# Kernel optimization log

Hardware: AMD Instinct MI355X
Metric: run time of the kernel (lower is better)

Reference implementation:

```python
import jax, jax.numpy as jnp
import numpy as np

D = 128      # d_model
H = 8        # n_heads
HD = D // H  # head_dim = 16
E = 256      # n_experts
R = 32       # kv_lora_rank
B, T = 4, 512
EPS = 1e-6


def _dense_init(k, fi, fo):
    s = float(1.0 / np.sqrt(fi))
    return jax.random.uniform(k, (fi, fo), minval=-s, maxval=s, dtype=jnp.float32)


def setup_inputs() -> dict:
    key = jax.random.key(0)
    ks = jax.random.split(key, 16)
    rng = np.random.RandomState(42)
    Q, _ = np.linalg.qr(rng.randn(D, D))
    glim = float(np.sqrt(6.0 / (D + D)))
    return {
        'x': jax.random.normal(ks[0], (B, T, D), dtype=jnp.float32),
        'g1': jnp.ones((D,), jnp.float32),
        'qW': _dense_init(ks[1], D, D), 'qb': jnp.zeros((D,), jnp.float32),
        'kdW': _dense_init(ks[2], D, R), 'kdb': jnp.zeros((R,), jnp.float32),
        'kuW': _dense_init(ks[3], R, 2 * D), 'kub': jnp.zeros((2 * D,), jnp.float32),
        'oW': _dense_init(ks[4], D, D), 'ob': jnp.zeros((D,), jnp.float32),
        'rot': jnp.asarray(Q, jnp.float32),
        'tq_scale': jnp.ones((D,), jnp.float32),
        's1W': _dense_init(ks[5], D, D), 's1b': jnp.zeros((D,), jnp.float32),
        's2W': _dense_init(ks[6], D, D), 's2b': jnp.zeros((D,), jnp.float32),
        'g2': jnp.ones((D,), jnp.float32),
        'gateW': _dense_init(ks[7], D, E), 'gateb': jnp.zeros((E,), jnp.float32),
        'expW': jax.random.uniform(ks[8], (E, D, D), minval=-glim, maxval=glim, dtype=jnp.float32),
        'm1W': _dense_init(ks[9], D, D), 'm1b': jnp.zeros((D,), jnp.float32),
        'm2W': _dense_init(ks[10], D, D), 'm2b': jnp.zeros((D,), jnp.float32),
    }


def _rmsnorm(x, g):
    return g * (x / jnp.sqrt(jnp.mean(x * x, axis=-1, keepdims=True) + EPS))


def _swiglu(x, w1, b1, w2, b2):
    gate = x @ w1 + b1
    return gate * jax.nn.sigmoid(gate) * (x @ w2 + b2)


def _mla(x, qW, qb, kdW, kdb, kuW, kub, oW, ob):
    b, t = x.shape[0], x.shape[1]
    q = (x @ qW + qb).reshape(b, t, H, HD)
    kv = ((x @ kdW + kdb) @ kuW + kub).reshape(b, t, H, 2 * HD)
    k, v = jnp.split(kv, 2, axis=-1)
    q = jax.nn.elu(q) + 1.0
    k = jax.nn.elu(k) + 1.0
    # linear attention: context[b,h,d,e] = sum_t k[b,t,h,d] v[b,t,h,e]
    context = jnp.einsum('bthd,bthe->bhde', k, v)
    out = jnp.einsum('bthd,bhde->bthe', q, context)
    k_sum = jnp.sum(k, axis=1)  # [b,h,d]
    z = 1.0 / (jnp.einsum('bthd,bhd->bth', q, k_sum) + EPS)
    out = out * z[..., None]
    return out.reshape(b, t, D) @ oW + ob


def _turbo_quant(x, rot, scale):
    x = x @ rot
    mag = jnp.sqrt(jnp.mean(x * x, axis=-1, keepdims=True) + EPS)
    phase = x / mag
    qp = jnp.clip(phase * 127.0, -127.0, 127.0) / 127.0
    phase = jax.lax.stop_gradient(qp - phase) + phase  # straight-through
    return phase * mag * scale


def _moe(h, gateW, gateb, expW, m1W, m1b, m2W, m2b):
    gate_scores = jax.nn.softmax(h @ gateW + gateb, axis=-1)  # [B,T,E]
    top_vals, top_idx = jax.lax.top_k(gate_scores, 2)
    top_w = top_vals / (jnp.sum(top_vals, axis=-1, keepdims=True) + EPS)
    # dense all-expert compute as in the original module
    eo = jnp.einsum('btd,edo->bteo', h, expW)  # [B,T,E,D]
    mask = jnp.sum(jax.nn.one_hot(top_idx, E, dtype=h.dtype) * top_w[..., None], axis=2)  # [B,T,E]
    wavg = jnp.einsum('bteo,bte->bto', eo, mask)
    wavg = _swiglu(wavg, m1W, m1b, m2W, m2b)
    diff_sq = jnp.square(eo - wavg[:, :, None, :])
    wvar = jnp.einsum('bteo,bte->bto', diff_sq, mask)
    consensus = jnp.exp(-jnp.mean(wvar, axis=-1))  # [B,T]
    return wavg, consensus


def reference(x, g1, qW, qb, kdW, kdb, kuW, kub, oW, ob, rot, tq_scale,
              s1W, s1b, s2W, s2b, g2, gateW, gateb, expW, m1W, m1b, m2W, m2b):
    attn_out = _turbo_quant(_mla(_rmsnorm(x, g1), qW, qb, kdW, kdb, kuW, kub, oW, ob), rot, tq_scale)
    x = x + _swiglu(attn_out, s1W, s1b, s2W, s2b)
    moe_out, consensus = _moe(_rmsnorm(x, g2), gateW, gateb, expW, m1W, m1b, m2W, m2b)
    return x + moe_out, consensus
```

## Files before the change

### kernel.cpp

```cpp
#include <hip/hip_runtime.h>
#include <math.h>

static constexpr int Dd    = 128;
static constexpr int NH    = 8;
static constexpr int NE    = 256;
static constexpr int RR    = 32;
static constexpr int TT    = 512;
static constexpr int NTOK  = 2048;
static constexpr int SLOTS = 256;
#define EPSF 1e-6f

static constexpr int FD_CTX   = 0;
static constexpr int FD_ROUTE = 4;
static constexpr int FD_EXP   = 5;
static constexpr int NFLAGS   = 261;

__device__ __forceinline__ float elu1(float v) { return v > 0.f ? v + 1.f : expf(v); }
__device__ __forceinline__ float sigm(float v) { return 1.f / (1.f + expf(-v)); }

__device__ __forceinline__ void flag_add(int* p) {
  __hip_atomic_fetch_add(p, 1, __ATOMIC_RELEASE, __HIP_MEMORY_SCOPE_AGENT);
}
__device__ __forceinline__ void flag_wait(int* p, int tgt) {
  int c = 0;
  while (__hip_atomic_load(p, __ATOMIC_ACQUIRE, __HIP_MEMORY_SCOPE_AGENT) < tgt) {
    __builtin_amdgcn_s_sleep(2);
    if (++c > (1 << 27)) break;
  }
}

__global__ __launch_bounds__(512) void k_pre(
    const float* __restrict__ x, const float* __restrict__ g1,
    const float* __restrict__ qW, const float* __restrict__ qb,
    const float* __restrict__ kdW, const float* __restrict__ kdb,
    const float* __restrict__ kuW, const float* __restrict__ kub,
    const float* __restrict__ oW, const float* __restrict__ ob,
    const float* __restrict__ rot,
    float* __restrict__ qbuf, float* __restrict__ kvbuf,
    float* __restrict__ ctx, float* __restrict__ ksum,
    int* __restrict__ cnt, int* __restrict__ flags,
    float* __restrict__ oR, float* __restrict__ bR) {
  const int tid = threadIdx.x;
  const int bid = blockIdx.x;
  const int j = tid & 127, g = tid >> 7;
  const int lane = tid & 63;
  const int n0 = bid * 4;

  __shared__ float4 h1T[128];
  __shared__ float4 part[3][128];
  __shared__ float4 kpart[8][32];
  __shared__ float4 kdT[32];
  __shared__ float4 kupart[256];
  __shared__ float4 rtmp[2];

  if (bid == 0) {
    for (int i = tid; i < 32 * 256; i += 512) ctx[i] = 0.f;
    ksum[tid] = 0.f;
    if (tid < NE) cnt[tid] = 0;
    if (tid < NFLAGS) flags[tid] = 0;
  }

  float xv[4];
  if (tid < 128) {
    float v[4];
#pragma unroll
    for (int t = 0; t < 4; t++) { xv[t] = x[(n0 + t) * Dd + j]; v[t] = xv[t] * xv[t]; }
#pragma unroll
    for (int o = 32; o > 0; o >>= 1) {
#pragma unroll
      for (int t = 0; t < 4; t++) v[t] += __shfl_xor(v[t], o, 64);
    }
    if (lane == 0) rtmp[tid >> 6] = make_float4(v[0], v[1], v[2], v[3]);
  }
  __syncthreads();
  if (tid < 128) {
    float g1j = g1[j];
#pragma unroll
    for (int t = 0; t < 4; t++) {
      float ss = ((const float*)&rtmp[0])[t] + ((const float*)&rtmp[1])[t];
      ((float*)&h1T[j])[t] = g1j * xv[t] * rsqrtf(ss * (1.f / 128.f) + EPSF);
    }
  }
  __syncthreads();

  {
    float a0 = 0, a1 = 0, a2 = 0, a3 = 0;
    const float* Wp = qW + (g * 32) * Dd + j;
#pragma unroll 16
    for (int i = 0; i < 32; i++) {
      float4 h4 = h1T[g * 32 + i];
      float w = Wp[i * Dd];
      a0 += h4.x * w; a1 += h4.y * w; a2 += h4.z * w; a3 += h4.w * w;
    }
    if (g) part[g - 1][j] = make_float4(a0, a1, a2, a3);
    __syncthreads();
    if (g == 0) {
      float4 p0 = part[0][j], p1 = part[1][j], p2 = part[2][j];
      float bb = qb[j];
      qbuf[(n0 + 0) * Dd + j] = elu1(a0 + p0.x + p1.x + p2.x + bb);
      qbuf[(n0 + 1) * Dd + j] = elu1(a1 + p0.y + p1.y + p2.y + bb);
      qbuf[(n0 + 2) * Dd + j] = elu1(a2 + p0.z + p1.z + p2.z + bb);
      qbuf[(n0 + 3) * Dd + j] = elu1(a3 + p0.w + p1.w + p2.w + bb);
    }
    __syncthreads();
  }

  if (tid < 256) {
    int col = tid & 31, ksp = tid >> 5;
    float a0 = 0, a1 = 0, a2 = 0, a3 = 0;
    const float* Wp = kdW + (ksp * 16) * RR + col;
#pragma unroll
    for (int i = 0; i < 16; i++) {
      float4 h4 = h1T[ksp * 16 + i];
      float w = Wp[i * RR];
      a0 += h4.x * w; a1 += h4.y * w; a2 += h4.z * w; a3 += h4.w * w;
    }
    kpart[ksp][col] = make_float4(a0, a1, a2, a3);
  }
  __syncthreads();
  if (tid < 32) {
    float bb = kdb[tid];
    float s0 = bb, s1 = bb, s2 = bb, s3 = bb;
#pragma unroll
    for (int k = 0; k < 8; k++) {
      float4 p = kpart[k][tid];
      s0 += p.x; s1 += p.y; s2 += p.z; s3 += p.w;
    }
    kdT[tid] = make_float4(s0, s1, s2, s3);
  }
  __syncthreads();

  {
    int col = tid & 255, kh = tid >> 8;
    float a0 = 0, a1 = 0, a2 = 0, a3 = 0;
    const float* Wp = kuW + (kh * 16) * 256 + col;
#pragma unroll
    for (int r = 0; r < 16; r++) {
      float4 k4 = kdT[kh * 16 + r];
      float w = Wp[r * 256];
      a0 += k4.x * w; a1 += k4.y * w; a2 += k4.z * w; a3 += k4.w * w;
    }
    if (kh) kupart[col] = make_float4(a0, a1, a2, a3);
    __syncthreads();
    if (!kh) {
      float4 p = kupart[col];
      float bb = kub[col];
      bool isk = (col & 31) < 16;
      float v0 = a0 + p.x + bb, v1 = a1 + p.y + bb, v2 = a2 + p.z + bb, v3 = a3 + p.w + bb;
      kvbuf[(n0 + 0) * 256 + col] = isk ? elu1(v0) : v0;
      kvbuf[(n0 + 1) * 256 + col] = isk ? elu1(v1) : v1;
      kvbuf[(n0 + 2) * 256 + col] = isk ? elu1(v2) : v2;
      kvbuf[(n0 + 3) * 256 + col] = isk ? elu1(v3) : v3;
    }
  }

  if (bid < 32) {
    int idx = bid * 512 + tid;
    int row = idx >> 7, col = idx & 127;
    const float* ow = oW + row * 128;
    float acc = 0.f;
#pragma unroll 8
    for (int k = 0; k < 128; k++) acc += ow[k] * rot[k * 128 + col];
    oR[idx] = acc;
  } else if (bid == 32 && tid < 128) {
    float acc = 0.f;
#pragma unroll 8
    for (int k = 0; k < 128; k++) acc += ob[k] * rot[k * 128 + tid];
    bR[tid] = acc;
  }
}

struct RParams {
  const float *x, *qbuf, *kvbuf, *oR, *bR, *tqs;
  const float *s1W, *s1b, *s2W, *s2b, *g2, *gateW, *gateb, *expW;
  const float *m1W, *m1b, *m2W, *m2b;
  float *ctx, *ksum, *h2buf, *ybuf, *out;
  int *cnt, *slottok, *flags;
};

__global__ __launch_bounds__(512, 4) void k_rest(RParams P) {
  const int tid = threadIdx.x;
  const int bid = blockIdx.x;
  const int j = tid & 127, g = tid >> 7;
  const int lane = tid & 63;
  const int n0 = bid * 4;
  const int b = bid >> 7;

  __shared__ float sh[64 * 32];
  __shared__ float4 bufA[128], bufB[128];
  __shared__ float4 part[3][128];
  __shared__ float4 gpart[256];
  __shared__ float4 rtmp[2];
  __shared__ float wvS[4][4]; __shared__ int wiS[4][4];
  __shared__ float zS[4][4];
  __shared__ int sE[4][2]; __shared__ int sSlot[4][2]; __shared__ float sWt[4][2];
  __shared__ __align__(16) float hT[128 * 20];
  __shared__ float4 y1T[128], y2T[128], inT[128], sT[128];

  float xres[4];
  if (tid < 128) {
#pragma unroll
    for (int t = 0; t < 4; t++) xres[t] = P.x[(n0 + t) * Dd + j];
  }
  ((float*)&bufA[j])[g] = P.qbuf[(n0 + g) * Dd + j];

  if (bid < 256) {
    const int bh = bid >> 3, c = bid & 7;
    const int bb = bh >> 3, h = bh & 7;
#pragma unroll
    for (int r = 0; r < 4; r++) {
      int lin = r * 512 + tid;
      int tok = lin >> 5, off = lin & 31;
      sh[lin] = P.kvbuf[((bb * TT + c * 64 + tok) * 256) + h * 32 + off];
    }
    __syncthreads();
    if (tid < 256) {
      const int d = tid >> 4, e = tid & 15;
      float acc = 0.f, ks = 0.f;
#pragma unroll 4
      for (int t = 0; t < 64; t++) {
        float kk = sh[t * 32 + d];
        acc += kk * sh[t * 32 + 16 + e];
        ks += kk;
      }
      atomicAdd(&P.ctx[bh * 256 + d * 16 + e], acc);
      if (e == 0) atomicAdd(&P.ksum[bh * 16 + d], ks);
    }
    __threadfence();
    __syncthreads();
    if (tid == 0) flag_add(&P.flags[FD_CTX + bb]);
  }

  if (tid == 0) flag_wait(&P.flags[FD_CTX + b], 64);
  __syncthreads();
  __threadfence();

  if (tid < 128) {
    int h = j >> 4, e = j & 15;
    const float* cpt = P.ctx + (b * NH + h) * 256;
    const float* kpt = P.ksum + (b * NH + h) * 16;
    float num[4] = {0, 0, 0, 0}, den[4] = {0, 0, 0, 0};
#pragma unroll
    for (int d = 0; d < 16; d++) {
      float cx = cpt[d * 16 + e], ks = kpt[d];
      float4 q4 = bufA[h * 16 + d];
      num[0] += q4.x * cx; num[1] += q4.y * cx; num[2] += q4.z * cx; num[3] += q4.w * cx;
      den[0] += q4.x * ks; den[1] += q4.y * ks; den[2] += q4.z * ks; den[3] += q4.w * ks;
    }
#pragma unroll
    for (int t = 0; t < 4; t++) ((float*)&bufB[j])[t] = num[t] / (den[t] + EPSF);
  }
  __syncthreads();

  {
    float a0 = 0, a1 = 0, a2 = 0, a3 = 0;
    const float* Wp = P.oR + (g * 32) * Dd + j;
#pragma unroll 16
    for (int i = 0; i < 32; i++) {
      float4 h4 = bufB[g * 32 + i];
      float w = Wp[i * Dd];
      a0 += h4.x * w; a1 += h4.y * w; a2 += h4.z * w; a3 += h4.w * w;
    }
    if (g) part[g - 1][j] = make_float4(a0, a1, a2, a3);
    __syncthreads();
    float tot[4];
    if (g == 0) {
      float4 p0 = part[0][j], p1 = part[1][j], p2 = part[2][j];
      float bb = P.bR[j];
      tot[0] = a0 + p0.x + p1.x + p2.x + bb; tot[1] = a1 + p0.y + p1.y + p2.y + bb;
      tot[2] = a2 + p0.z + p1.z + p2.z + bb; tot[3] = a3 + p0.w + p1.w + p2.w + bb;
      float v[4];
#pragma unroll
      for (int t = 0; t < 4; t++) v[t] = tot[t] * tot[t];
#pragma unroll
      for (int o = 32; o > 0; o >>= 1) {
#pragma unroll
        for (int t = 0; t < 4; t++) v[t] += __shfl_xor(v[t], o, 64);
      }
      if (lane == 0) rtmp[tid >> 6] = make_float4(v[0], v[1], v[2], v[3]);
    }
    __syncthreads();
    if (g == 0) {
      float scj = P.tqs[j];
#pragma unroll
      for (int t = 0; t < 4; t++) {
        float ss = ((const float*)&rtmp[0])[t] + ((const float*)&rtmp[1])[t];
        float mag = sqrtf(ss * (1.f / 128.f) + EPSF);
        float zc = fminf(fmaxf(tot[t], -mag), mag);
        ((float*)&bufA[j])[t] = zc * scj;
      }
    }
    __syncthreads();
  }

  float xn[4] = {0.f, 0.f, 0.f, 0.f};
  {
    float a0 = 0, a1 = 0, a2 = 0, a3 = 0;
    const float* Wp = (g < 2 ? P.s1W : P.s2W) + ((g & 1) * 64) * Dd + j;
#pragma unroll 16
    for (int i = 0; i < 64; i++) {
      float4 h4 = bufA[(g & 1) * 64 + i];
      float w = Wp[i * Dd];
      a0 += h4.x * w; a1 += h4.y * w; a2 += h4.z * w; a3 += h4.w * w;
    }
    if (g) part[g - 1][j] = make_float4(a0, a1, a2, a3);
    __syncthreads();
    if (g == 0) {
      float b1 = P.s1b[j], b2 = P.s2b[j];
      float4 p0 = part[0][j], p1 = part[1][j], p2 = part[2][j];
      float gv[4], uv[4], v[4];
      gv[0] = a0 + p0.x + b1; gv[1] = a1 + p0.y + b1;
      gv[2] = a2 + p0.z + b1; gv[3] = a3 + p0.w + b1;
      uv[0] = p1.x + p2.x + b2; uv[1] = p1.y + p2.y + b2;
      uv[2] = p1.z + p2.z + b2; uv[3] = p1.w + p2.w + b2;
      float g2j = P.g2[j];
#pragma unroll
      for (int t = 0; t < 4; t++) {
        xn[t] = xres[t] + gv[t] * sigm(gv[t]) * uv[t];
        ((float*)&bufB[j])[t] = g2j * xn[t];
        v[t] = xn[t] * xn[t];
      }
#pragma unroll
      for (int o = 32; o > 0; o >>= 1) {
#pragma unroll
        for (int t = 0; t < 4; t++) v[t] += __shfl_xor(v[t], o, 64);
      }
      if (lane == 0) rtmp[tid >> 6] = make_float4(v[0], v[1], v[2], v[3]);
    }
    __syncthreads();
  }

  float val[4]; float r2v[4];
  {
    int col = tid & 255, kh = tid >> 8;
    float a0 = 0, a1 = 0, a2 = 0, a3 = 0;
    const float* Wp = P.gateW + (kh * 64) * NE + col;
#pragma unroll 16
    for (int i = 0; i < 64; i++) {
      float4 h4 = bufB[kh * 64 + i];
      float w = Wp[i * NE];
      a0 += h4.x * w; a1 += h4.y * w; a2 += h4.z * w; a3 += h4.w * w;
    }
    if (kh) gpart[col] = make_float4(a0, a1, a2, a3);
    __syncthreads();
#pragma unroll
    for (int t = 0; t < 4; t++) {
      float ss = ((const float*)&rtmp[0])[t] + ((const float*)&rtmp[1])[t];
      r2v[t] = rsqrtf(ss * (1.f / 128.f) + EPSF);
    }
    if (!kh) {
      float4 p = gpart[col];
      float bb = P.gateb[col];
      val[0] = (a0 + p.x) * r2v[0] + bb; val[1] = (a1 + p.y) * r2v[1] + bb;
      val[2] = (a2 + p.z) * r2v[2] + bb; val[3] = (a3 + p.w) * r2v[3] + bb;
    }
    if (tid < 128) {
#pragma unroll
      for (int t = 0; t < 4; t++)
        P.h2buf[(n0 + t) * Dd + j] = ((const float*)&bufB[j])[t] * r2v[t];
    }
  }
  __syncthreads();

  float m1[4]; int i1[4];
  {
    if (tid < 256) {
      float bv[4]; int bi[4];
#pragma unroll
      for (int t = 0; t < 4; t++) { bv[t] = val[t]; bi[t] = tid; }
#pragma unroll
      for (int o = 32; o > 0; o >>= 1) {
#pragma unroll
        for (int t = 0; t < 4; t++) {
          float wv = __shfl_xor(bv[t], o, 64);
          int wi = __shfl_xor(bi[t], o, 64);
          if (wv > bv[t] || (wv == bv[t] && wi < bi[t])) { bv[t] = wv; bi[t] = wi; }
        }
      }
      if (lane == 0) {
#pragma unroll
        for (int t = 0; t < 4; t++) { wvS[tid >> 6][t] = bv[t]; wiS[tid >> 6][t] = bi[t]; }
      }
    }
    __syncthreads();
    if (tid < 256) {
#pragma unroll
// ... 34 lines not shown
    __syncthreads();
    if (tid < 256) {
#pragma unroll
      for (int t = 0; t < 4; t++) {
        m2[t] = wvS[0][t]; i2[t] = wiS[0][t];
#pragma unroll
        for (int w = 1; w < 4; w++) {
          float cv = wvS[w][t]; int ci = wiS[w][t];
          if (cv > m2[t] || (cv == m2[t] && ci < i2[t])) { m2[t] = cv; i2[t] = ci; }
        }
      }
    }
    __syncthreads();
  }
  {
    if (tid < 256) {
      float v[4];
#pragma unroll
      for (int t = 0; t < 4; t++) v[t] = expf(val[t] - m1[t]);
#pragma unroll
      for (int o = 32; o > 0; o >>= 1) {
#pragma unroll
        for (int t = 0; t < 4; t++) v[t] += __shfl_xor(v[t], o, 64);
      }
      if (lane == 0) {
#pragma unroll
        for (int t = 0; t < 4; t++) zS[tid >> 6][t] = v[t];
      }
    }
    __syncthreads();
  }
  if (tid < 4) {
    int t = tid, tok = n0 + t;
    float Z = zS[0][t] + zS[1][t] + zS[2][t] + zS[3][t];
    float p1 = 1.f / Z;
    float p2 = expf(m2[t] - m1[t]) / Z;
    float s = p1 + p2 + EPSF;
    int e1 = i1[t], e2 = i2[t];
    int s1 = atomicAdd(&P.cnt[e1], 1); if (s1 > SLOTS - 1) s1 = SLOTS - 1;
    int s2 = atomicAdd(&P.cnt[e2], 1); if (s2 > SLOTS - 1) s2 = SLOTS - 1;
    int sl1 = e1 * SLOTS + s1, sl2 = e2 * SLOTS + s2;
    P.slottok[sl1] = tok; P.slottok[sl2] = tok;
    sE[t][0] = e1; sE[t][1] = e2;
    sSlot[t][0] = sl1; sSlot[t][1] = sl2;
    sWt[t][0] = p1 / s; sWt[t][1] = p2 / s;
  }

  __threadfence();
  __syncthreads();
  if (tid == 0) {
    flag_add(&P.flags[FD_ROUTE]);
    flag_wait(&P.flags[FD_ROUTE], 512);
  }
  __syncthreads();
  __threadfence();

  {
    const int e = bid >> 1, sub = bid & 1;
    int n = __hip_atomic_load(&P.cnt[e], __ATOMIC_RELAXED, __HIP_MEMORY_SCOPE_AGENT);
    if (n > SLOTS) n = SLOTS;
    const int base = e * SLOTS;
    const float* Wp = P.expW + (size_t)e * Dd * Dd + j;
    for (int t0 = sub * 16; t0 < n; t0 += 32) {
      int m = n - t0; if (m > 16) m = 16;
      __syncthreads();
      for (int tt = g; tt < m; tt += 4) {
        int tok = P.slottok[base + t0 + tt];
        hT[j * 20 + tt] = P.h2buf[tok * Dd + j];
      }
      __syncthreads();
      float acc[4] = {0, 0, 0, 0};
#pragma unroll 8
      for (int i = 0; i < 128; i++) {
        float w = Wp[i * Dd];
        float4 h4 = *(const float4*)&hT[i * 20 + g * 4];
        acc[0] += h4.x * w; acc[1] += h4.y * w; acc[2] += h4.z * w; acc[3] += h4.w * w;
      }
#pragma unroll
      for (int k = 0; k < 4; k++) {
        int tt = g * 4 + k;
        if (tt < m) P.ybuf[(size_t)(base + t0 + tt) * Dd + j] = acc[k];
      }
    }
    __threadfence();
    __syncthreads();
    if (tid == 0) flag_add(&P.flags[FD_EXP + e]);
  }

  if (tid < 8) {
    int t = tid >> 1, sl = tid & 1;
    flag_wait(&P.flags[FD_EXP + sE[t][sl]], 2);
  }
  __syncthreads();
  __threadfence();

  {
    float y1 = P.ybuf[(size_t)sSlot[g][0] * Dd + j];
    float y2 = P.ybuf[(size_t)sSlot[g][1] * Dd + j];
    ((float*)&y1T[j])[g] = y1;
    ((float*)&y2T[j])[g] = y2;
    ((float*)&inT[j])[g] = sWt[g][0] * y1 + sWt[g][1] * y2;
  }
  __syncthreads();

  {
    float a0 = 0, a1 = 0, a2 = 0, a3 = 0;
    const float* Wp = (g < 2 ? P.m1W : P.m2W) + ((g & 1) * 64) * Dd + j;
#pragma unroll 16
    for (int i = 0; i < 64; i++) {
      float4 h4 = inT[(g & 1) * 64 + i];
      float w = Wp[i * Dd];
      a0 += h4.x * w; a1 += h4.y * w; a2 += h4.z * w; a3 += h4.w * w;
    }
    if (g) part[g - 1][j] = make_float4(a0, a1, a2, a3);
    __syncthreads();
    if (g == 0) {
      float b1 = P.m1b[j], b2 = P.m2b[j];
      float4 p0 = part[0][j], p1 = part[1][j], p2 = part[2][j];
      float gv[4], uv[4];
      gv[0] = a0 + p0.x + b1; gv[1] = a1 + p0.y + b1;
      gv[2] = a2 + p0.z + b1; gv[3] = a3 + p0.w + b1;
      uv[0] = p1.x + p2.x + b2; uv[1] = p1.y + p2.y + b2;
      uv[2] = p1.z + p2.z + b2; uv[3] = p1.w + p2.w + b2;
#pragma unroll
      for (int t = 0; t < 4; t++) {
        float sv = gv[t] * sigm(gv[t]) * uv[t];
        ((float*)&sT[j])[t] = sv;
        P.out[(n0 + t) * Dd + j] = xn[t] + sv;
      }
    }
    __syncthreads();
  }

  if (tid < 128) {
    float v[4];
#pragma unroll
    for (int t = 0; t < 4; t++) {
      float sv = ((const float*)&sT[j])[t];
      float d1 = ((const float*)&y1T[j])[t] - sv;
      float d2 = ((const float*)&y2T[j])[t] - sv;
      v[t] = sWt[t][0] * d1 * d1 + sWt[t][1] * d2 * d2;
    }
#pragma unroll
    for (int o = 32; o > 0; o >>= 1) {
#pragma unroll
      for (int t = 0; t < 4; t++) v[t] += __shfl_xor(v[t], o, 64);
    }
    if (lane == 0) rtmp[tid >> 6] = make_float4(v[0], v[1], v[2], v[3]);
  }
  __syncthreads();
  if (tid < 4) {
    float s = ((const float*)&rtmp[0])[tid] + ((const float*)&rtmp[1])[tid];
    P.out[NTOK * Dd + n0 + tid] = expf(-s * (1.f / 128.f));
  }
}

__global__ __launch_bounds__(256) void k_ctx_fb(const float* __restrict__ kv,
                                                float* __restrict__ ctx,
                                                float* __restrict__ ksum) {
  const int blk = blockIdx.x;
  const int tid = threadIdx.x;
  const int bh = blk >> 3, c = blk & 7;
  const int b = bh >> 3, h = bh & 7;
  const int d = tid >> 4, e = tid & 15;
  __shared__ float sh[64 * 32];
#pragma unroll
  for (int r = 0; r < 8; r++) {
    int lin = r * 256 + tid;
    int tok = lin >> 5, off = lin & 31;
    sh[lin] = kv[((b * TT + c * 64 + tok) * 256) + h * 32 + off];
  }
  __syncthreads();
  float acc = 0.f, ks = 0.f;
#pragma unroll 4
  for (int t = 0; t < 64; t++) {
    float kk = sh[t * 32 + d];
    acc += kk * sh[t * 32 + 16 + e];
    ks += kk;
  }
  atomicAdd(&ctx[bh * 256 + d * 16 + e], acc);
  if (e == 0) atomicAdd(&ksum[bh * 16 + d], ks);
}

__global__ __launch_bounds__(512) void k_mid_fb(
    const float* __restrict__ x, const float* __restrict__ qbuf,
    const float* __restrict__ ctx, const float* __restrict__ ksum,
    const float* __restrict__ oR, const float* __restrict__ bR,
    const float* __restrict__ tqs,
    const float* __restrict__ s1W, const float* __restrict__ s1b,
    const float* __restrict__ s2W, const float* __restrict__ s2b,
    const float* __restrict__ g2, const float* __restrict__ gateW,
    const float* __restrict__ gateb,
    float* __restrict__ xnbuf, float* __restrict__ h2buf,
    float* __restrict__ gw, int* __restrict__ tokslot,
    int* __restrict__ slottok, int* __restrict__ cnt) {
  const int tid = threadIdx.x;
  const int j = tid & 127, g = tid >> 7;
  const int lane = tid & 63;
  const int n0 = blockIdx.x * 4;
  const int b = n0 >> 9;

  __shared__ float4 bufA[128], bufB[128];
  __shared__ float4 part[3][128];
  __shared__ float4 gpart[256];
  __shared__ float4 rtmp[2];
  __shared__ float wvS[4][4]; __shared__ int wiS[4][4];
  __shared__ float zS[4][4];

  float xres[4];
  if (tid < 128) {
#pragma unroll
    for (int t = 0; t < 4; t++) xres[t] = x[(n0 + t) * Dd + j];
  }
  ((float*)&bufA[j])[g] = qbuf[(n0 + g) * Dd + j];
  __syncthreads();

  if (tid < 128) {
    int h = j >> 4, e = j & 15;
    const float* cpt = ctx + (b * NH + h) * 256;
    const float* kpt = ksum + (b * NH + h) * 16;
    float num[4] = {0, 0, 0, 0}, den[4] = {0, 0, 0, 0};
#pragma unroll
    for (int d = 0; d < 16; d++) {
      float cx = cpt[d * 16 + e], ks = kpt[d];
      float4 q4 = bufA[h * 16 + d];
      num[0] += q4.x * cx; num[1] += q4.y * cx; num[2] += q4.z * cx; num[3] += q4.w * cx;
      den[0] += q4.x * ks; den[1] += q4.y * ks; den[2] += q4.z * ks; den[3] += q4.w * ks;
    }
#pragma unroll
    for (int t = 0; t < 4; t++) ((float*)&bufB[j])[t] = num[t] / (den[t] + EPSF);
  }
  __syncthreads();

  {
    float a0 = 0, a1 = 0, a2 = 0, a3 = 0;
    const float* Wp = oR + (g * 32) * Dd + j;
#pragma unroll 16
    for (int i = 0; i < 32; i++) {
      float4 h4 = bufB[g * 32 + i];
      float w = Wp[i * Dd];
      a0 += h4.x * w; a1 += h4.y * w; a2 += h4.z * w; a3 += h4.w * w;
    }
    if (g) part[g - 1][j] = make_float4(a0, a1, a2, a3);
    __syncthreads();
    float tot[4];
    if (g == 0) {
      float4 p0 = part[0][j], p1 = part[1][j], p2 = part[2][j];
      float bb = bR[j];
      tot[0] = a0 + p0.x + p1.x + p2.x + bb; tot[1] = a1 + p0.y + p1.y + p2.y + bb;
      tot[2] = a2 + p0.z + p1.z + p2.z + bb; tot[3] = a3 + p0.w + p1.w + p2.w + bb;
      float v[4];
#pragma unroll
      for (int t = 0; t < 4; t++) v[t] = tot[t] * tot[t];
#pragma unroll
      for (int o = 32; o > 0; o >>= 1) {
#pragma unroll
        for (int t = 0; t < 4; t++) v[t] += __shfl_xor(v[t], o, 64);
      }
      if (lane == 0) rtmp[tid >> 6] = make_float4(v[0], v[1], v[2], v[3]);
    }
    __syncthreads();
    if (g == 0) {
      float scj = tqs[j];
#pragma unroll
      for (int t = 0; t < 4; t++) {
        float ss = ((const float*)&rtmp[0])[t] + ((const float*)&rtmp[1])[t];
        float mag = sqrtf(ss * (1.f / 128.f) + EPSF);
        float zc = fminf(fmaxf(tot[t], -mag), mag);
        ((float*)&bufA[j])[t] = zc * scj;
      }
    }
    __syncthreads();
  }

  {
    float a0 = 0, a1 = 0, a2 = 0, a3 = 0;
    const float* Wp = (g < 2 ? s1W : s2W) + ((g & 1) * 64) * Dd + j;
#pragma unroll 16
    for (int i = 0; i < 64; i++) {
      float4 h4 = bufA[(g & 1) * 64 + i];
      float w = Wp[i * Dd];
      a0 += h4.x * w; a1 += h4.y * w; a2 += h4.z * w; a3 += h4.w * w;
    }
    if (g) part[g - 1][j] = make_float4(a0, a1, a2, a3);
    __syncthreads();
    if (g == 0) {
      float b1 = s1b[j], b2 = s2b[j];
      float4 p0 = part[0][j], p1 = part[1][j], p2 = part[2][j];
      float gv[4], uv[4], xn[4], v[4];
      gv[0] = a0 + p0.x + b1; gv[1] = a1 + p0.y + b1;
      gv[2] = a2 + p0.z + b1; gv[3] = a3 + p0.w + b1;
      uv[0] = p1.x + p2.x + b2; uv[1] = p1.y + p2.y + b2;
      uv[2] = p1.z + p2.z + b2; uv[3] = p1.w + p2.w + b2;
      float g2j = g2[j];
#pragma unroll
      for (int t = 0; t < 4; t++) {
        xn[t] = xres[t] + gv[t] * sigm(gv[t]) * uv[t];
        xnbuf[(n0 + t) * Dd + j] = xn[t];
        ((float*)&bufB[j])[t] = g2j * xn[t];
        v[t] = xn[t] * xn[t];
      }
#pragma unroll
      for (int o = 32; o > 0; o >>= 1) {
#pragma unroll
        for (int t = 0; t < 4; t++) v[t] += __shfl_xor(v[t], o, 64);
      }
// ... 144 lines not shown
                                                const int* __restrict__ cnt,
                                                const float* __restrict__ expW,
                                                float* __restrict__ ybuf) {
  const int e = blockIdx.x >> 1, sub = blockIdx.x & 1;
  int n = cnt[e]; if (n > SLOTS) n = SLOTS;
  const int base = e * SLOTS;
  const int tid = threadIdx.x;
  const int j = tid & 127, g = tid >> 7;
  __shared__ __align__(16) float hT[128 * 20];
  const float* Wp = expW + (size_t)e * Dd * Dd + j;
  for (int t0 = sub * 16; t0 < n; t0 += 32) {
    int m = n - t0; if (m > 16) m = 16;
    __syncthreads();
    for (int tt = g; tt < m; tt += 4) {
      int tok = slottok[base + t0 + tt];
      hT[j * 20 + tt] = h2buf[tok * Dd + j];
    }
    __syncthreads();
    float acc[4] = {0, 0, 0, 0};
#pragma unroll 8
    for (int i = 0; i < 128; i++) {
      float w = Wp[i * Dd];
      float4 h4 = *(const float4*)&hT[i * 20 + g * 4];
      acc[0] += h4.x * w; acc[1] += h4.y * w; acc[2] += h4.z * w; acc[3] += h4.w * w;
    }
#pragma unroll
    for (int k = 0; k < 4; k++) {
      int tt = g * 4 + k;
      if (tt < m) ybuf[(size_t)(base + t0 + tt) * Dd + j] = acc[k];
    }
  }
}

__global__ __launch_bounds__(512) void k_post_fb(
    const float* __restrict__ xnbuf, const float* __restrict__ ybuf,
    const int* __restrict__ tokslot, const float* __restrict__ gw,
    const float* __restrict__ m1W, const float* __restrict__ m1b,
    const float* __restrict__ m2W, const float* __restrict__ m2b,
    float* __restrict__ out) {
  const int tid = threadIdx.x;
  const int j = tid & 127, g = tid >> 7;
  const int lane = tid & 63;
  const int n0 = blockIdx.x * 4;

  __shared__ float4 y1T[128], y2T[128], inT[128], sT[128];
  __shared__ float4 part[3][128];
  __shared__ float4 rtmp[2];
  __shared__ int sSlot[4][2];
  __shared__ float sWt[4][2];

  if (tid < 4) {
    sSlot[tid][0] = tokslot[(n0 + tid) * 2];
    sSlot[tid][1] = tokslot[(n0 + tid) * 2 + 1];
    sWt[tid][0] = gw[(n0 + tid) * 2];
    sWt[tid][1] = gw[(n0 + tid) * 2 + 1];
  }
  __syncthreads();

  {
    float y1 = ybuf[(size_t)sSlot[g][0] * Dd + j];
    float y2 = ybuf[(size_t)sSlot[g][1] * Dd + j];
    ((float*)&y1T[j])[g] = y1;
    ((float*)&y2T[j])[g] = y2;
    ((float*)&inT[j])[g] = sWt[g][0] * y1 + sWt[g][1] * y2;
  }
  __syncthreads();

  {
    float a0 = 0, a1 = 0, a2 = 0, a3 = 0;
    const float* Wp = (g < 2 ? m1W : m2W) + ((g & 1) * 64) * Dd + j;
#pragma unroll 16
    for (int i = 0; i < 64; i++) {
      float4 h4 = inT[(g & 1) * 64 + i];
      float w = Wp[i * Dd];
      a0 += h4.x * w; a1 += h4.y * w; a2 += h4.z * w; a3 += h4.w * w;
    }
    if (g) part[g - 1][j] = make_float4(a0, a1, a2, a3);
    __syncthreads();
    if (g == 0) {
      float b1 = m1b[j], b2 = m2b[j];
      float4 p0 = part[0][j], p1 = part[1][j], p2 = part[2][j];
      float gv[4], uv[4];
      gv[0] = a0 + p0.x + b1; gv[1] = a1 + p0.y + b1;
      gv[2] = a2 + p0.z + b1; gv[3] = a3 + p0.w + b1;
      uv[0] = p1.x + p2.x + b2; uv[1] = p1.y + p2.y + b2;
      uv[2] = p1.z + p2.z + b2; uv[3] = p1.w + p2.w + b2;
#pragma unroll
      for (int t = 0; t < 4; t++) {
        float sv = gv[t] * sigm(gv[t]) * uv[t];
        ((float*)&sT[j])[t] = sv;
        out[(n0 + t) * Dd + j] = xnbuf[(n0 + t) * Dd + j] + sv;
      }
    }
    __syncthreads();
  }

  if (tid < 128) {
    float v[4];
#pragma unroll
    for (int t = 0; t < 4; t++) {
      float sv = ((const float*)&sT[j])[t];
      float d1 = ((const float*)&y1T[j])[t] - sv;
      float d2 = ((const float*)&y2T[j])[t] - sv;
      v[t] = sWt[t][0] * d1 * d1 + sWt[t][1] * d2 * d2;
    }
#pragma unroll
    for (int o = 32; o > 0; o >>= 1) {
#pragma unroll
      for (int t = 0; t < 4; t++) v[t] += __shfl_xor(v[t], o, 64);
    }
    if (lane == 0) rtmp[tid >> 6] = make_float4(v[0], v[1], v[2], v[3]);
  }
  __syncthreads();
  if (tid < 4) {
    float s = ((const float*)&rtmp[0])[tid] + ((const float*)&rtmp[1])[tid];
    out[NTOK * Dd + n0 + tid] = expf(-s * (1.f / 128.f));
  }
}

extern "C" void kernel_launch(void* const* d_in, const int* in_sizes, int n_in,
                              void* d_out, int out_size, void* d_ws, size_t ws_size,
                              hipStream_t stream) {
  const float* x   = (const float*)d_in[0];
  const float* g1  = (const float*)d_in[1];
  const float* qW  = (const float*)d_in[2];
  const float* qb  = (const float*)d_in[3];
  const float* kdW = (const float*)d_in[4];
  const float* kdb = (const float*)d_in[5];
  const float* kuW = (const float*)d_in[6];
  const float* kub = (const float*)d_in[7];
  const float* oW  = (const float*)d_in[8];
  const float* ob  = (const float*)d_in[9];
  const float* rot = (const float*)d_in[10];
  const float* tqs = (const float*)d_in[11];
  const float* s1W = (const float*)d_in[12];
  const float* s1b = (const float*)d_in[13];
  const float* s2W = (const float*)d_in[14];
  const float* s2b = (const float*)d_in[15];
  const float* g2  = (const float*)d_in[16];
  const float* gW  = (const float*)d_in[17];
  const float* gb  = (const float*)d_in[18];
  const float* eW  = (const float*)d_in[19];
  const float* m1W = (const float*)d_in[20];
  const float* m1b = (const float*)d_in[21];
  const float* m2W = (const float*)d_in[22];
  const float* m2b = (const float*)d_in[23];
  float* out = (float*)d_out;
  float* ws  = (float*)d_ws;

  float* ctx     = ws;
  float* ksum    = ws + 8192;
  float* oR      = ws + 8704;
  float* bR      = ws + 25088;
  float* qbuf    = ws + 25216;
  float* kvbuf   = ws + 287360;
  float* h2buf   = ws + 811648;
  float* ybuf    = ws + 1073792;
  int*   cnt     = (int*)(ws + 9462400);
  int*   slottok = (int*)(ws + 9462656);
  int*   flags   = (int*)(ws + 9528192);
  float* xnbuf   = ws + 9528576;
  float* gw      = ws + 9790720;
  int*   tokslot = (int*)(ws + 9794816);

  k_pre<<<NTOK / 4, 512, 0, stream>>>(x, g1, qW, qb, kdW, kdb, kuW, kub,
                                      oW, ob, rot, qbuf, kvbuf, ctx, ksum,
                                      cnt, flags, oR, bR);

  RParams p;
  p.x = x; p.qbuf = qbuf; p.kvbuf = kvbuf; p.oR = oR; p.bR = bR; p.tqs = tqs;
  p.s1W = s1W; p.s1b = s1b; p.s2W = s2W; p.s2b = s2b; p.g2 = g2;
  p.gateW = gW; p.gateb = gb; p.expW = eW;
  p.m1W = m1W; p.m1b = m1b; p.m2W = m2W; p.m2b = m2b;
  p.ctx = ctx; p.ksum = ksum; p.h2buf = h2buf; p.ybuf = ybuf; p.out = out;
  p.cnt = cnt; p.slottok = slottok; p.flags = flags;

  void* args[] = {(void*)&p};
  hipError_t err = hipErrorUnknown;
  int nb = 0;
  if (hipOccupancyMaxActiveBlocksPerMultiprocessor(
          &nb, reinterpret_cast<const void*>(&k_rest), 512, 0) == hipSuccess &&
      nb >= 2) {
    err = hipLaunchCooperativeKernel((void*)k_rest, dim3(NTOK / 4), dim3(512),
                                     args, 0u, stream);
  }
  if (err == hipSuccess) return;

  k_ctx_fb<<<256, 256, 0, stream>>>(kvbuf, ctx, ksum);
  k_mid_fb<<<NTOK / 4, 512, 0, stream>>>(x, qbuf, ctx, ksum, oR, bR, tqs,
                                         s1W, s1b, s2W, s2b, g2, gW, gb,
                                         xnbuf, h2buf, gw, tokslot, slottok, cnt);
  k_exp_fb<<<NE * 2, 512, 0, stream>>>(h2buf, slottok, cnt, eW, ybuf);
  k_post_fb<<<NTOK / 4, 512, 0, stream>>>(xnbuf, ybuf, tokslot, gw,
                                          m1W, m1b, m2W, m2b, out);
}
```

Measured before the change: 162.5 us.

## Fuse pre-attention projection kernel into cooperative persistent kernel with flag sync

Merges the separate pre-kernel (RMSNorm, q/kv projections, oW·rot precompute) into the cooperative main kernel. q stays in shared memory instead of round-tripping through global memory. The kv context reduction moves from 256 blocks using atomics to 32 blocks that each wait on a per-batch flag and loop over all 8 chunks. Flags and counters are now zeroed with a memset. This removes one kernel launch and its global-memory handoff, at the cost of serialising the context computation onto fewer blocks and adding spin-waits on new flags.

```diff
diff --git a/kernel.cpp b/kernel.cpp
--- a/kernel.cpp
+++ b/kernel.cpp
@@ -10,10 +10,12 @@
 static constexpr int SLOTS = 256;
 #define EPSF 1e-6f
 
-static constexpr int FD_CTX   = 0;
-static constexpr int FD_ROUTE = 4;
-static constexpr int FD_EXP   = 5;
-static constexpr int NFLAGS   = 261;
+static constexpr int FK_KV    = 0;
+static constexpr int FD_CTX   = 4;
+static constexpr int FD_OR    = 8;
+static constexpr int FD_ROUTE = 9;
+static constexpr int FD_EXP   = 10;
+static constexpr int NFLAGS   = 266;
 
 __device__ __forceinline__ float elu1(float v) { return v > 0.f ? v + 1.f : expf(v); }
 __device__ __forceinline__ float sigm(float v) { return 1.f / (1.f + expf(-v)); }
@@ -29,156 +31,15 @@
   }
 }
 
-__global__ __launch_bounds__(512) void k_pre(
-    const float* __restrict__ x, const float* __restrict__ g1,
-    const float* __restrict__ qW, const float* __restrict__ qb,
-    const float* __restrict__ kdW, const float* __restrict__ kdb,
-    const float* __restrict__ kuW, const float* __restrict__ kub,
-    const float* __restrict__ oW, const float* __restrict__ ob,
-    const float* __restrict__ rot,
-    float* __restrict__ qbuf, float* __restrict__ kvbuf,
-    float* __restrict__ ctx, float* __restrict__ ksum,
-    int* __restrict__ cnt, int* __restrict__ flags,
-    float* __restrict__ oR, float* __restrict__ bR) {
-  const int tid = threadIdx.x;
-  const int bid = blockIdx.x;
-  const int j = tid & 127, g = tid >> 7;
-  const int lane = tid & 63;
-  const int n0 = bid * 4;
-
-  __shared__ float4 h1T[128];
-  __shared__ float4 part[3][128];
-  __shared__ float4 kpart[8][32];
-  __shared__ float4 kdT[32];
-  __shared__ float4 kupart[256];
-  __shared__ float4 rtmp[2];
-
-  if (bid == 0) {
-    for (int i = tid; i < 32 * 256; i += 512) ctx[i] = 0.f;
-    ksum[tid] = 0.f;
-    if (tid < NE) cnt[tid] = 0;
-    if (tid < NFLAGS) flags[tid] = 0;
-  }
-
-  float xv[4];
-  if (tid < 128) {
-    float v[4];
-#pragma unroll
-    for (int t = 0; t < 4; t++) { xv[t] = x[(n0 + t) * Dd + j]; v[t] = xv[t] * xv[t]; }
-#pragma unroll
-    for (int o = 32; o > 0; o >>= 1) {
-#pragma unroll
-      for (int t = 0; t < 4; t++) v[t] += __shfl_xor(v[t], o, 64);
-    }
-    if (lane == 0) rtmp[tid >> 6] = make_float4(v[0], v[1], v[2], v[3]);
-  }
-  __syncthreads();
-  if (tid < 128) {
-    float g1j = g1[j];
-#pragma unroll
-    for (int t = 0; t < 4; t++) {
-      float ss = ((const float*)&rtmp[0])[t] + ((const float*)&rtmp[1])[t];
-      ((float*)&h1T[j])[t] = g1j * xv[t] * rsqrtf(ss * (1.f / 128.f) + EPSF);
-    }
-  }
-  __syncthreads();
-
-  {
-    float a0 = 0, a1 = 0, a2 = 0, a3 = 0;
-    const float* Wp = qW + (g * 32) * Dd + j;
-#pragma unroll 16
-    for (int i = 0; i < 32; i++) {
-      float4 h4 = h1T[g * 32 + i];
-      float w = Wp[i * Dd];
-      a0 += h4.x * w; a1 += h4.y * w; a2 += h4.z * w; a3 += h4.w * w;
-    }
-    if (g) part[g - 1][j] = make_float4(a0, a1, a2, a3);
-    __syncthreads();
-    if (g == 0) {
-      float4 p0 = part[0][j], p1 = part[1][j], p2 = part[2][j];
-      float bb = qb[j];
-      qbuf[(n0 + 0) * Dd + j] = elu1(a0 + p0.x + p1.x + p2.x + bb);
-      qbuf[(n0 + 1) * Dd + j] = elu1(a1 + p0.y + p1.y + p2.y + bb);
-      qbuf[(n0 + 2) * Dd + j] = elu1(a2 + p0.z + p1.z + p2.z + bb);
-      qbuf[(n0 + 3) * Dd + j] = elu1(a3 + p0.w + p1.w + p2.w + bb);
-    }
-    __syncthreads();
-  }
-
-  if (tid < 256) {
-    int col = tid & 31, ksp = tid >> 5;
-    float a0 = 0, a1 = 0, a2 = 0, a3 = 0;
-    const float* Wp = kdW + (ksp * 16) * RR + col;
-#pragma unroll
-    for (int i = 0; i < 16; i++) {
-      float4 h4 = h1T[ksp * 16 + i];
-      float w = Wp[i * RR];
-      a0 += h4.x * w; a1 += h4.y * w; a2 += h4.z * w; a3 += h4.w * w;
-    }
-    kpart[ksp][col] = make_float4(a0, a1, a2, a3);
-  }
-  __syncthreads();
-  if (tid < 32) {
-    float bb = kdb[tid];
-    float s0 = bb, s1 = bb, s2 = bb, s3 = bb;
-#pragma unroll
-    for (int k = 0; k < 8; k++) {
-      float4 p = kpart[k][tid];
-      s0 += p.x; s1 += p.y; s2 += p.z; s3 += p.w;
-    }
-    kdT[tid] = make_float4(s0, s1, s2, s3);
-  }
-  __syncthreads();
-
-  {
-    int col = tid & 255, kh = tid >> 8;
-    float a0 = 0, a1 = 0, a2 = 0, a3 = 0;
-    const float* Wp = kuW + (kh * 16) * 256 + col;
-#pragma unroll
-    for (int r = 0; r < 16; r++) {
-      float4 k4 = kdT[kh * 16 + r];
-      float w = Wp[r * 256];
-      a0 += k4.x * w; a1 += k4.y * w; a2 += k4.z * w; a3 += k4.w * w;
-    }
-    if (kh) kupart[col] = make_float4(a0, a1, a2, a3);
-    __syncthreads();
-    if (!kh) {
-      float4 p = kupart[col];
-      float bb = kub[col];
-      bool isk = (col & 31) < 16;
-      float v0 = a0 + p.x + bb, v1 = a1 + p.y + bb, v2 = a2 + p.z + bb, v3 = a3 + p.w + bb;
-      kvbuf[(n0 + 0) * 256 + col] = isk ? elu1(v0) : v0;
-      kvbuf[(n0 + 1) * 256 + col] = isk ? elu1(v1) : v1;
-      kvbuf[(n0 + 2) * 256 + col] = isk ? elu1(v2) : v2;
-      kvbuf[(n0 + 3) * 256 + col] = isk ? elu1(v3) : v3;
-    }
-  }
-
-  if (bid < 32) {
-    int idx = bid * 512 + tid;
-    int row = idx >> 7, col = idx & 127;
-    const float* ow = oW + row * 128;
-    float acc = 0.f;
-#pragma unroll 8
-    for (int k = 0; k < 128; k++) acc += ow[k] * rot[k * 128 + col];
-    oR[idx] = acc;
-  } else if (bid == 32 && tid < 128) {
-    float acc = 0.f;
-#pragma unroll 8
-    for (int k = 0; k < 128; k++) acc += ob[k] * rot[k * 128 + tid];
-    bR[tid] = acc;
-  }
-}
-
-struct RParams {
-  const float *x, *qbuf, *kvbuf, *oR, *bR, *tqs;
+struct AParams {
+  const float *x, *g1, *qW, *qb, *kdW, *kdb, *kuW, *kub, *oW, *ob, *rot, *tqs;
   const float *s1W, *s1b, *s2W, *s2b, *g2, *gateW, *gateb, *expW;
   const float *m1W, *m1b, *m2W, *m2b;
-  float *ctx, *ksum, *h2buf, *ybuf, *out;
+  float *kvbuf, *ctx, *ksum, *oR, *bR, *h2buf, *ybuf, *out;
   int *cnt, *slottok, *flags;
 };
 
-__global__ __launch_bounds__(512, 4) void k_rest(RParams P) {
+__global__ __launch_bounds__(512, 4) void k_all(AParams P) {
   const int tid = threadIdx.x;
   const int bid = blockIdx.x;
   const int j = tid & 127, g = tid >> 7;
@@ -197,41 +58,167 @@
   __shared__ __align__(16) float hT[128 * 20];
   __shared__ float4 y1T[128], y2T[128], inT[128], sT[128];
 
+  float4* kpart4 = (float4*)hT;
+  float4* kdT4   = (float4*)(hT + 1024);
+
   float xres[4];
+  {
+    float v[4];
+    if (tid < 128) {
+#pragma unroll
+      for (int t = 0; t < 4; t++) { xres[t] = P.x[(n0 + t) * Dd + j]; v[t] = xres[t] * xres[t]; }
+#pragma unroll
+      for (int o = 32; o > 0; o >>= 1) {
+#pragma unroll
+        for (int t = 0; t < 4; t++) v[t] += __shfl_xor(v[t], o, 64);
+      }
+      if (lane == 0) rtmp[tid >> 6] = make_float4(v[0], v[1], v[2], v[3]);
+    }
+  }
+  __syncthreads();
   if (tid < 128) {
-#pragma unroll
-    for (int t = 0; t < 4; t++) xres[t] = P.x[(n0 + t) * Dd + j];
-  }
-  ((float*)&bufA[j])[g] = P.qbuf[(n0 + g) * Dd + j];
-
-  if (bid < 256) {
-    const int bh = bid >> 3, c = bid & 7;
-    const int bb = bh >> 3, h = bh & 7;
-#pragma unroll
-    for (int r = 0; r < 4; r++) {
-      int lin = r * 512 + tid;
-      int tok = lin >> 5, off = lin & 31;
-      sh[lin] = P.kvbuf[((bb * TT + c * 64 + tok) * 256) + h * 32 + off];
-    }
-    __syncthreads();
+    float g1j = P.g1[j];
+#pragma unroll
+    for (int t = 0; t < 4; t++) {
+      float ss = ((const float*)&rtmp[0])[t] + ((const float*)&rtmp[1])[t];
+      ((float*)&bufB[j])[t] = g1j * xres[t] * rsqrtf(ss * (1.f / 128.f) + EPSF);
+    }
+  }
+  __syncthreads();
+
+  {
+    float a0 = 0, a1 = 0, a2 = 0, a3 = 0;
+    const float* Wp = P.qW + (g * 32) * Dd + j;
+#pragma unroll 16
+    for (int i = 0; i < 32; i++) {
+      float4 h4 = bufB[g * 32 + i];
+      float w = Wp[i * Dd];
+      a0 += h4.x * w; a1 += h4.y * w; a2 += h4.z * w; a3 += h4.w * w;
+    }
+    if (g) part[g - 1][j] = make_float4(a0, a1, a2, a3);
+    __syncthreads();
+    if (g == 0) {
+      float4 p0 = part[0][j], p1 = part[1][j], p2 = part[2][j];
+      float bb = P.qb[j];
+      ((float*)&bufA[j])[0] = elu1(a0 + p0.x + p1.x + p2.x + bb);
+      ((float*)&bufA[j])[1] = elu1(a1 + p0.y + p1.y + p2.y + bb);
+      ((float*)&bufA[j])[2] = elu1(a2 + p0.z + p1.z + p2.z + bb);
+      ((float*)&bufA[j])[3] = elu1(a3 + p0.w + p1.w + p2.w + bb);
+    }
+    __syncthreads();
+  }
+
+  if (tid < 256) {
+    int col = tid & 31, ksp = tid >> 5;
+    float a0 = 0, a1 = 0, a2 = 0, a3 = 0;
+    const float* Wp = P.kdW + (ksp * 16) * RR + col;
+#pragma unroll
+    for (int i = 0; i < 16; i++) {
+      float4 h4 = bufB[ksp * 16 + i];
+      float w = Wp[i * RR];
+      a0 += h4.x * w; a1 += h4.y * w; a2 += h4.z * w; a3 += h4.w * w;
+    }
+    kpart4[ksp * 32 + col] = make_float4(a0, a1, a2, a3);
+  }
+  __syncthreads();
+  if (tid < 32) {
+    float bb = P.kdb[tid];
+    float s0 = bb, s1 = bb, s2 = bb, s3 = bb;
+#pragma unroll
+    for (int k = 0; k < 8; k++) {
+      float4 p = kpart4[k * 32 + tid];
+      s0 += p.x; s1 += p.y; s2 += p.z; s3 += p.w;
+    }
+    kdT4[tid] = make_float4(s0, s1, s2, s3);
+  }
+  __syncthreads();
+
+  {
+    int col = tid & 255, kh = tid >> 8;
+    float a0 = 0, a1 = 0, a2 = 0, a3 = 0;
+    const float* Wp = P.kuW + (kh * 16) * 256 + col;
+#pragma unroll
+    for (int r = 0; r < 16; r++) {
+      float4 k4 = kdT4[kh * 16 + r];
+      float w = Wp[r * 256];
+      a0 += k4.x * w; a1 += k4.y * w; a2 += k4.z * w; a3 += k4.w * w;
+    }
+    if (kh) gpart[col] = make_float4(a0, a1, a2, a3);
+    __syncthreads();
+    if (!kh) {
+      float4 p = gpart[col];
+      float bb = P.kub[col];
+      bool isk = (col & 31) < 16;
+      float v0 = a0 + p.x + bb, v1 = a1 + p.y + bb, v2 = a2 + p.z + bb, v3 = a3 + p.w + bb;
+      P.kvbuf[(n0 + 0) * 256 + col] = isk ? elu1(v0) : v0;
+      P.kvbuf[(n0 + 1) * 256 + col] = isk ? elu1(v1) : v1;
+      P.kvbuf[(n0 + 2) * 256 + col] = isk ? elu1(v2) : v2;
+      P.kvbuf[(n0 + 3) * 256 + col] = isk ? elu1(v3) : v3;
+    }
+  }
+  __threadfence();
+  __syncthreads();
+  if (tid == 0) flag_add(&P.flags[FK_KV + b]);
+
+  if (bid < 32) {
+    int idx = bid * 512 + tid;
+    int row = idx >> 7, col = idx & 127;
+    const float* ow = P.oW + row * 128;
+    float acc = 0.f;
+#pragma unroll 8
+    for (int k = 0; k < 128; k++) acc += ow[k] * P.rot[k * 128 + col];
+    P.oR[idx] = acc;
+    __threadfence();
+    __syncthreads();
+    if (tid == 0) flag_add(&P.flags[FD_OR]);
+  } else if (bid == 32) {
+    if (tid < 128) {
+      float acc = 0.f;
+#pragma unroll 8
+      for (int k = 0; k < 128; k++) acc += P.ob[k] * P.rot[k * 128 + tid];
+      P.bR[tid] = acc;
+    }
+    __threadfence();
+    __syncthreads();
+    if (tid == 0) flag_add(&P.flags[FD_OR]);
+  }
+
+  if (bid < 32) {
+    const int bh = bid, bb = bh >> 3, h = bh & 7;
+    if (tid == 0) flag_wait(&P.flags[FK_KV + bb], 128);
+    __syncthreads();
+    __threadfence();
+    float acc = 0.f, ks = 0.f;
+    const int d = tid >> 4, e = tid & 15;
+    for (int c = 0; c < 8; c++) {
+      __syncthreads();
+#pragma unroll
+      for (int r = 0; r < 4; r++) {
+        int lin = r * 512 + tid;
+        int tok = lin >> 5, off = lin & 31;
+        sh[lin] = P.kvbuf[((bb * TT + c * 64 + tok) * 256) + h * 32 + off];
+      }
+      __syncthreads();
+      if (tid < 256) {
+#pragma unroll 4
+        for (int t = 0; t < 64; t++) {
+          float kk = sh[t * 32 + d];
+          acc += kk * sh[t * 32 + 16 + e];
+          ks += kk;
+        }
+      }
+    }
     if (tid < 256) {
-      const int d = tid >> 4, e = tid & 15;
-      float acc = 0.f, ks = 0.f;
-#pragma unroll 4
-      for (int t = 0; t < 64; t++) {
-        float kk = sh[t * 32 + d];
-        acc += kk * sh[t * 32 + 16 + e];
-        ks += kk;
-      }
-      atomicAdd(&P.ctx[bh * 256 + d * 16 + e], acc);
-      if (e == 0) atomicAdd(&P.ksum[bh * 16 + d], ks);
+      P.ctx[bh * 256 + d * 16 + e] = acc;
+      if (e == 0) P.ksum[bh * 16 + d] = ks;
     }
     __threadfence();
     __syncthreads();
     if (tid == 0) flag_add(&P.flags[FD_CTX + bb]);
   }
 
-  if (tid == 0) flag_wait(&P.flags[FD_CTX + b], 64);
+  if (tid == 0) flag_wait(&P.flags[FD_CTX + b], 8);
+  if (tid == 1) flag_wait(&P.flags[FD_OR], 33);
   __syncthreads();
   __threadfence();
 
@@ -572,6 +559,146 @@
   if (tid < 4) {
     float s = ((const float*)&rtmp[0])[tid] + ((const float*)&rtmp[1])[tid];
     P.out[NTOK * Dd + n0 + tid] = expf(-s * (1.f / 128.f));
+  }
+}
+
+__global__ __launch_bounds__(512) void k_pre_fb(
+    const float* __restrict__ x, const float* __restrict__ g1,
+    const float* __restrict__ qW, const float* __restrict__ qb,
+    const float* __restrict__ kdW, const float* __restrict__ kdb,
+    const float* __restrict__ kuW, const float* __restrict__ kub,
+    const float* __restrict__ oW, const float* __restrict__ ob,
+    const float* __restrict__ rot,
+    float* __restrict__ qbuf, float* __restrict__ kvbuf,
+    float* __restrict__ ctx, float* __restrict__ ksum,
+    int* __restrict__ cnt,
+    float* __restrict__ oR, float* __restrict__ bR) {
+  const int tid = threadIdx.x;
+  const int bid = blockIdx.x;
+  const int j = tid & 127, g = tid >> 7;
+  const int lane = tid & 63;
+  const int n0 = bid * 4;
+
+  __shared__ float4 h1T[128];
+  __shared__ float4 part[3][128];
+  __shared__ float4 kpart[8][32];
+  __shared__ float4 kdT[32];
+  __shared__ float4 kupart[256];
+  __shared__ float4 rtmp[2];
+
+  if (bid == 0) {
+    for (int i = tid; i < 32 * 256; i += 512) ctx[i] = 0.f;
+    ksum[tid] = 0.f;
+    if (tid < NE) cnt[tid] = 0;
+  }
+
+  float xv[4];
+  if (tid < 128) {
+    float v[4];
+#pragma unroll
+    for (int t = 0; t < 4; t++) { xv[t] = x[(n0 + t) * Dd + j]; v[t] = xv[t] * xv[t]; }
+#pragma unroll
+    for (int o = 32; o > 0; o >>= 1) {
+#pragma unroll
+      for (int t = 0; t < 4; t++) v[t] += __shfl_xor(v[t], o, 64);
+    }
+    if (lane == 0) rtmp[tid >> 6] = make_float4(v[0], v[1], v[2], v[3]);
+  }
+  __syncthreads();
+  if (tid < 128) {
+    float g1j = g1[j];
+#pragma unroll
+    for (int t = 0; t < 4; t++) {
+      float ss = ((const float*)&rtmp[0])[t] + ((const float*)&rtmp[1])[t];
+      ((float*)&h1T[j])[t] = g1j * xv[t] * rsqrtf(ss * (1.f / 128.f) + EPSF);
+    }
+  }
+  __syncthreads();
+
+  {
+    float a0 = 0, a1 = 0, a2 = 0, a3 = 0;
+    const float* Wp = qW + (g * 32) * Dd + j;
+#pragma unroll 16
+    for (int i = 0; i < 32; i++) {
+      float4 h4 = h1T[g * 32 + i];
+      float w = Wp[i * Dd];
+      a0 += h4.x * w; a1 += h4.y * w; a2 += h4.z * w; a3 += h4.w * w;
+    }
+    if (g) part[g - 1][j] = make_float4(a0, a1, a2, a3);
+    __syncthreads();
+    if (g == 0) {
+      float4 p0 = part[0][j], p1 = part[1][j], p2 = part[2][j];
+      float bb = qb[j];
+      qbuf[(n0 + 0) * Dd + j] = elu1(a0 + p0.x + p1.x + p2.x + bb);
+      qbuf[(n0 + 1) * Dd + j] = elu1(a1 + p0.y + p1.y + p2.y + bb);
+      qbuf[(n0 + 2) * Dd + j] = elu1(a2 + p0.z + p1.z + p2.z + bb);
+      qbuf[(n0 + 3) * Dd + j] = elu1(a3 + p0.w + p1.w + p2.w + bb);
+    }
+    __syncthreads();
+  }
+
+  if (tid < 256) {
+    int col = tid & 31, ksp = tid >> 5;
+    float a0 = 0, a1 = 0, a2 = 0, a3 = 0;
+    const float* Wp = kdW + (ksp * 16) * RR + col;
+#pragma unroll
+    for (int i = 0; i < 16; i++) {
+      float4 h4 = h1T[ksp * 16 + i];
+      float w = Wp[i * RR];
+      a0 += h4.x * w; a1 += h4.y * w; a2 += h4.z * w; a3 += h4.w * w;
+    }
+    kpart[ksp][col] = make_float4(a0, a1, a2, a3);
+  }
+  __syncthreads();
+  if (tid < 32) {
+    float bb = kdb[tid];
+    float s0 = bb, s1 = bb, s2 = bb, s3 = bb;
+#pragma unroll
+    for (int k = 0; k < 8; k++) {
+      float4 p = kpart[k][tid];
+      s0 += p.x; s1 += p.y; s2 += p.z; s3 += p.w;
+    }
+    kdT[tid] = make_float4(s0, s1, s2, s3);
+  }
+  __syncthreads();
+
+  {
+    int col = tid & 255, kh = tid >> 8;
+    float a0 = 0, a1 = 0, a2 = 0, a3 = 0;
+    const float* Wp = kuW + (kh * 16) * 256 + col;
+#pragma unroll
+    for (int r = 0; r < 16; r++) {
+      float4 k4 = kdT[kh * 16 + r];
+      float w = Wp[r * 256];
+      a0 += k4.x * w; a1 += k4.y * w; a2 += k4.z * w; a3 += k4.w * w;
+    }
+    if (kh) kupart[col] = make_float4(a0, a1, a2, a3);
+    __syncthreads();
+    if (!kh) {
+      float4 p = kupart[col];
+      float bb = kub[col];
+      bool isk = (col & 31) < 16;
+      float v0 = a0 + p.x + bb, v1 = a1 + p.y + bb, v2 = a2 + p.z + bb, v3 = a3 + p.w + bb;
+      kvbuf[(n0 + 0) * 256 + col] = isk ? elu1(v0) : v0;
+      kvbuf[(n0 + 1) * 256 + col] = isk ? elu1(v1) : v1;
+      kvbuf[(n0 + 2) * 256 + col] = isk ? elu1(v2) : v2;
+      kvbuf[(n0 + 3) * 256 + col] = isk ? elu1(v3) : v3;
+    }
+  }
+
+  if (bid < 32) {
+    int idx = bid * 512 + tid;
+    int row = idx >> 7, col = idx & 127;
+    const float* ow = oW + row * 128;
+    float acc = 0.f;
+#pragma unroll 8
+    for (int k = 0; k < 128; k++) acc += ow[k] * rot[k * 128 + col];
+    oR[idx] = acc;
+  } else if (bid == 32 && tid < 128) {
+    float acc = 0.f;
+#pragma unroll 8
+    for (int k = 0; k < 128; k++) acc += ob[k] * rot[k * 128 + tid];
+    bR[tid] = acc;
   }
 }
 
@@ -1022,40 +1149,43 @@
   float* ksum    = ws + 8192;
   float* oR      = ws + 8704;
   float* bR      = ws + 25088;
-  float* qbuf    = ws + 25216;
-  float* kvbuf   = ws + 287360;
-  float* h2buf   = ws + 811648;
-  float* ybuf    = ws + 1073792;
-  int*   cnt     = (int*)(ws + 9462400);
-  int*   slottok = (int*)(ws + 9462656);
-  int*   flags   = (int*)(ws + 9528192);
-  float* xnbuf   = ws + 9528576;
-  float* gw      = ws + 9790720;
-  int*   tokslot = (int*)(ws + 9794816);
-
-  k_pre<<<NTOK / 4, 512, 0, stream>>>(x, g1, qW, qb, kdW, kdb, kuW, kub,
-                                      oW, ob, rot, qbuf, kvbuf, ctx, ksum,
-                                      cnt, flags, oR, bR);
-
-  RParams p;
-  p.x = x; p.qbuf = qbuf; p.kvbuf = kvbuf; p.oR = oR; p.bR = bR; p.tqs = tqs;
+  float* kvbuf   = ws + 25216;
+  float* h2buf   = ws + 549504;
+  float* ybuf    = ws + 811648;
+  int*   slottok = (int*)(ws + 9200256);
+  int*   cnt     = (int*)(ws + 9265792);
+  int*   flags   = (int*)(ws + 9266048);
+  float* qbuf    = ws + 9266560;
+  float* xnbuf   = ws + 9528704;
+  float* gw      = ws + 9790848;
+  int*   tokslot = (int*)(ws + 9794944);
+
+  hipMemsetAsync(cnt, 0, (256 + 512) * sizeof(int), stream);
+
+  AParams p;
+  p.x = x; p.g1 = g1; p.qW = qW; p.qb = qb; p.kdW = kdW; p.kdb = kdb;
+  p.kuW = kuW; p.kub = kub; p.oW = oW; p.ob = ob; p.rot = rot; p.tqs = tqs;
   p.s1W = s1W; p.s1b = s1b; p.s2W = s2W; p.s2b = s2b; p.g2 = g2;
   p.gateW = gW; p.gateb = gb; p.expW = eW;
   p.m1W = m1W; p.m1b = m1b; p.m2W = m2W; p.m2b = m2b;
-  p.ctx = ctx; p.ksum = ksum; p.h2buf = h2buf; p.ybuf = ybuf; p.out = out;
+  p.kvbuf = kvbuf; p.ctx = ctx; p.ksum = ksum; p.oR = oR; p.bR = bR;
+  p.h2buf = h2buf; p.ybuf = ybuf; p.out = out;
   p.cnt = cnt; p.slottok = slottok; p.flags = flags;
 
   void* args[] = {(void*)&p};
   hipError_t err = hipErrorUnknown;
   int nb = 0;
   if (hipOccupancyMaxActiveBlocksPerMultiprocessor(
-          &nb, reinterpret_cast<const void*>(&k_rest), 512, 0) == hipSuccess &&
+          &nb, reinterpret_cast<const void*>(&k_all), 512, 0) == hipSuccess &&
       nb >= 2) {
-    err = hipLaunchCooperativeKernel((void*)k_rest, dim3(NTOK / 4), dim3(512),
+    err = hipLaunchCooperativeKernel((void*)k_all, dim3(NTOK / 4), dim3(512),
                                      args, 0u, stream);
   }
   if (err == hipSuccess) return;
 
+  k_pre_fb<<<NTOK / 4, 512, 0, stream>>>(x, g1, qW, qb, kdW, kdb, kuW, kub,
+                                         oW, ob, rot, qbuf, kvbuf, ctx, ksum,
+                                         cnt, oR, bR);
   k_ctx_fb<<<256, 256, 0, stream>>>(kvbuf, ctx, ksum);
   k_mid_fb<<<NTOK / 4, 512, 0, stream>>>(x, qbuf, ctx, ksum, oR, bR, tqs,
                                          s1W, s1b, s2W, s2b, g2, gW, gb,
```

Result: no change. 163.2 us (+0.4%).
